# Kernel optimization log

Hardware: AMD Instinct MI355X
Metric: run time of the kernel (lower is better)

The kernel has to match this reference:

```python
import jax, jax.numpy as jnp
import numpy as np

SCORE_THRESHOLD = 0.35
TARGET_CLASS_ID = 0.0
R = 4_194_304  # number of candidate detections (rois)


def setup_inputs() -> dict:
    key = jax.random.key(0)
    k1, k2, k3 = jax.random.split(key, 3)
    class_ids = jax.random.randint(k1, (R,), 0, 4).astype(jnp.float32)
    boxes = jax.random.uniform(k2, (R, 4), dtype=jnp.float32)
    scores = jax.random.uniform(k3, (R,), dtype=jnp.float32)
    detections = jnp.concatenate([class_ids[:, None], boxes, scores[:, None]], axis=1)[None]  # [1, R, 6]
    return {"detections": detections}


def _compact(data, mask):
    # Stable stream compaction with fixed output shape: valid rows moved to the
    # front (original order preserved), invalid tail zero-padded.
    # data: [R, D] float, mask: [R] bool  ->  ([R, D], n_valid)
    order = jnp.argsort(jnp.logical_not(mask), stable=True)  # valid (False-key) first
    sel = jnp.take(data, order, axis=0)
    n = jnp.sum(mask.astype(jnp.int32))
    keep = (jnp.arange(data.shape[0]) < n)[:, None]
    return jnp.where(keep, sel, jnp.zeros((), data.dtype)), n


def reference(detections):
    # detections: [1, R, 6] = [class_id, x1, y1, x2, y2, score]
    d = detections[0]
    class_ids = d[:, 0]
    scores = d[:, 5]
    valid = (class_ids == TARGET_CLASS_ID) & (scores >= SCORE_THRESHOLD)
    valid_full = scores >= SCORE_THRESHOLD

    sel, n = _compact(d, valid)
    # rois: zero class stub + xyxy (score dropped), [1, R, 5]; padded rows are all-zero
    rois = jnp.concatenate([jnp.zeros((d.shape[0], 1), d.dtype), sel[:, 1:5]], axis=1)[None]

    rois_full, n_full = _compact(d, valid_full)
    rois_full = rois_full[None]  # [1, R, 6]

    return rois, rois_full, n, n_full
```

## Files before the change

kernel.cpp:

```cpp
#include <hip/hip_runtime.h>

typedef unsigned int uint32;
typedef unsigned long long uint64;

#define BLOCK 256
#define IPT 16
#define CHUNK (BLOCK * IPT)
#define SCORE_THR 0.35f

__global__ void count_kernel(const float* __restrict__ det,
                             uint32* __restrict__ c0, uint32* __restrict__ c1,
                             int R) {
    int tid = threadIdx.x;
    long long base = (long long)blockIdx.x * CHUNK;
    uint32 cnt0 = 0, cnt1 = 0;
    for (int i = 0; i < IPT; ++i) {
        long long row = base + (long long)i * BLOCK + tid;
        if (row < R) {
            const float* p = det + row * 6;
            float c = p[0];
            float s = p[5];
            bool m1 = (s >= SCORE_THR);
            bool m0 = m1 && (c == 0.0f);
            cnt1 += m1 ? 1u : 0u;
            cnt0 += m0 ? 1u : 0u;
        }
    }
    for (int off = 32; off > 0; off >>= 1) {
        cnt0 += __shfl_down(cnt0, off, 64);
        cnt1 += __shfl_down(cnt1, off, 64);
    }
    __shared__ uint32 r0[BLOCK / 64], r1[BLOCK / 64];
    int wave = tid >> 6, lane = tid & 63;
    if (lane == 0) { r0[wave] = cnt0; r1[wave] = cnt1; }
    __syncthreads();
    if (tid == 0) {
        uint32 t0 = 0, t1 = 0;
        for (int w = 0; w < BLOCK / 64; ++w) { t0 += r0[w]; t1 += r1[w]; }
        c0[blockIdx.x] = t0;
        c1[blockIdx.x] = t1;
    }
}

__global__ void scan_kernel(const uint32* __restrict__ c0, const uint32* __restrict__ c1,
                            uint32* __restrict__ o0, uint32* __restrict__ o1,
                            uint32* __restrict__ totals, float* __restrict__ out_n,
                            int nb) {
    __shared__ uint32 s0[1024], s1[1024];
    int t = threadIdx.x;
    uint32 carry0 = 0, carry1 = 0;
    for (int basei = 0; basei < nb; basei += 1024) {
        int i = basei + t;
        uint32 v0 = (i < nb) ? c0[i] : 0u;
        uint32 v1 = (i < nb) ? c1[i] : 0u;
        s0[t] = v0; s1[t] = v1;
        __syncthreads();
        for (int d = 1; d < 1024; d <<= 1) {
            uint32 a0 = (t >= d) ? s0[t - d] : 0u;
            uint32 a1 = (t >= d) ? s1[t - d] : 0u;
            __syncthreads();
            s0[t] += a0; s1[t] += a1;
            __syncthreads();
        }
        if (i < nb) {
            o0[i] = carry0 + s0[t] - v0;
            o1[i] = carry1 + s1[t] - v1;
        }
        uint32 tot0 = carry0 + s0[1023];
        uint32 tot1 = carry1 + s1[1023];
        __syncthreads();
        carry0 = tot0; carry1 = tot1;
    }
    if (t == 0) {
        totals[0] = carry0;
        totals[1] = carry1;
        out_n[0] = (float)carry0;
        out_n[1] = (float)carry1;
    }
}

__global__ void scatter_kernel(const float* __restrict__ det,
                               float* __restrict__ rois, float* __restrict__ roisf,
                               const uint32* __restrict__ o0, const uint32* __restrict__ o1,
                               int R) {
    __shared__ uint32 wc0[BLOCK / 64], wc1[BLOCK / 64];
    __shared__ uint32 run0, run1;
    int tid = threadIdx.x;
    int wave = tid >> 6, lane = tid & 63;
    if (tid == 0) { run0 = o0[blockIdx.x]; run1 = o1[blockIdx.x]; }
    __syncthreads();
    long long base = (long long)blockIdx.x * CHUNK;
    for (int i = 0; i < IPT; ++i) {
        long long row = base + (long long)i * BLOCK + tid;
        bool m0 = false, m1 = false;
        float d0 = 0, d1 = 0, d2 = 0, d3 = 0, d4 = 0, d5 = 0;
        if (row < R) {
            const float* p = det + row * 6;
            d0 = p[0]; d1 = p[1]; d2 = p[2]; d3 = p[3]; d4 = p[4]; d5 = p[5];
            m1 = (d5 >= SCORE_THR);
            m0 = m1 && (d0 == 0.0f);
        }
        uint64 b0 = __ballot(m0);
        uint64 b1 = __ballot(m1);
        if (lane == 0) { wc0[wave] = (uint32)__popcll(b0); wc1[wave] = (uint32)__popcll(b1); }
        __syncthreads();
        uint32 wp0 = 0, wp1 = 0;
        for (int w = 0; w < wave; ++w) { wp0 += wc0[w]; wp1 += wc1[w]; }
        uint64 lt = (lane == 0) ? 0ull : ((1ull << lane) - 1ull);
        if (m0) {
            uint32 pos = run0 + wp0 + (uint32)__popcll(b0 & lt);
            float* q = rois + (long long)pos * 5;
            q[0] = 0.0f; q[1] = d1; q[2] = d2; q[3] = d3; q[4] = d4;
        }
        if (m1) {
            uint32 pos = run1 + wp1 + (uint32)__popcll(b1 & lt);
            float* q = roisf + (long long)pos * 6;
            q[0] = d0; q[1] = d1; q[2] = d2; q[3] = d3; q[4] = d4; q[5] = d5;
        }
        __syncthreads();
        if (tid == 0) {
            uint32 t0 = 0, t1 = 0;
            for (int w = 0; w < BLOCK / 64; ++w) { t0 += wc0[w]; t1 += wc1[w]; }
            run0 += t0; run1 += t1;
        }
        __syncthreads();
    }
}

__global__ void zero_kernel(float* __restrict__ rois, float* __restrict__ roisf,
                            const uint32* __restrict__ totals, long long R) {
    long long n0 = totals[0], n1 = totals[1];
    long long z0 = R * 5 - n0 * 5;
    long long z1 = R * 6 - n1 * 6;
    long long total = z0 + z1;
    long long idx = (long long)blockIdx.x * blockDim.x + threadIdx.x;
    long long stride = (long long)gridDim.x * blockDim.x;
    float* base0 = rois + n0 * 5;
    float* base1 = roisf + n1 * 6;
    for (long long k = idx; k < total; k += stride) {
        if (k < z0) base0[k] = 0.0f;
        else        base1[k - z0] = 0.0f;
    }
}

extern "C" void kernel_launch(void* const* d_in, const int* in_sizes, int n_in,
                              void* d_out, int out_size, void* d_ws, size_t ws_size,
                              hipStream_t stream) {
    const float* det = (const float*)d_in[0];
    float* out = (float*)d_out;
    int R = in_sizes[0] / 6;
    int NB = (R + CHUNK - 1) / CHUNK;

    uint32* ws = (uint32*)d_ws;
    uint32* c0 = ws;
    uint32* c1 = ws + NB;
    uint32* o0 = ws + 2 * NB;
    uint32* o1 = ws + 3 * NB;
    uint32* totals = ws + 4 * NB;

    float* rois  = out;
    float* roisf = out + (long long)R * 5;
    float* nout  = out + (long long)R * 11;

    count_kernel<<<NB, BLOCK, 0, stream>>>(det, c0, c1, R);
    scan_kernel<<<1, 1024, 0, stream>>>(c0, c1, o0, o1, totals, nout, NB);
    scatter_kernel<<<NB, BLOCK, 0, stream>>>(det, rois, roisf, o0, o1, R);
    zero_kernel<<<2048, BLOCK, 0, stream>>>(rois, roisf, totals, (long long)R);
}
```

Before: 290.9 us.

## Fuse scan, scatter and zero-fill into one kernel with float4 loads

Removes the single-block scan kernel and the separate zero kernel. Each scatter block now sums the per-block counts itself to get its prefix and the totals, then writes compacted rows and zero-fills its share of the padded tail. Both passes load rows as float4 triples covering two rows per thread, and the scatter loop uses double-buffered shared counters so it needs one barrier per iteration instead of three. In exchange, every block redundantly reads all NB counts (1024 blocks) and the zero-fill stride is now tied to the grid size.

```diff
diff --git a/kernel.cpp b/kernel.cpp
--- a/kernel.cpp
+++ b/kernel.cpp
@@ -7,6 +7,21 @@
 #define IPT 16
 #define CHUNK (BLOCK * IPT)
 #define SCORE_THR 0.35f
+
+__device__ inline void block_reduce2(uint32& a, uint32& b) {
+    int tid = threadIdx.x;
+    int wave = tid >> 6, lane = tid & 63;
+    for (int off = 32; off > 0; off >>= 1) {
+        a += __shfl_down(a, off, 64);
+        b += __shfl_down(b, off, 64);
+    }
+    __shared__ uint32 ra[BLOCK / 64], rb[BLOCK / 64];
+    if (lane == 0) { ra[wave] = a; rb[wave] = b; }
+    __syncthreads();
+    uint32 sa = 0, sb = 0;
+    for (int w = 0; w < BLOCK / 64; ++w) { sa += ra[w]; sb += rb[w]; }
+    a = sa; b = sb;
+}
 
 __global__ void count_kernel(const float* __restrict__ det,
                              uint32* __restrict__ c0, uint32* __restrict__ c1,
@@ -14,132 +29,172 @@
     int tid = threadIdx.x;
     long long base = (long long)blockIdx.x * CHUNK;
     uint32 cnt0 = 0, cnt1 = 0;
-    for (int i = 0; i < IPT; ++i) {
-        long long row = base + (long long)i * BLOCK + tid;
-        if (row < R) {
-            const float* p = det + row * 6;
-            float c = p[0];
-            float s = p[5];
-            bool m1 = (s >= SCORE_THR);
-            bool m0 = m1 && (c == 0.0f);
-            cnt1 += m1 ? 1u : 0u;
-            cnt0 += m0 ? 1u : 0u;
-        }
-    }
-    for (int off = 32; off > 0; off >>= 1) {
-        cnt0 += __shfl_down(cnt0, off, 64);
-        cnt1 += __shfl_down(cnt1, off, 64);
-    }
-    __shared__ uint32 r0[BLOCK / 64], r1[BLOCK / 64];
-    int wave = tid >> 6, lane = tid & 63;
-    if (lane == 0) { r0[wave] = cnt0; r1[wave] = cnt1; }
-    __syncthreads();
-    if (tid == 0) {
-        uint32 t0 = 0, t1 = 0;
-        for (int w = 0; w < BLOCK / 64; ++w) { t0 += r0[w]; t1 += r1[w]; }
-        c0[blockIdx.x] = t0;
-        c1[blockIdx.x] = t1;
-    }
-}
-
-__global__ void scan_kernel(const uint32* __restrict__ c0, const uint32* __restrict__ c1,
-                            uint32* __restrict__ o0, uint32* __restrict__ o1,
-                            uint32* __restrict__ totals, float* __restrict__ out_n,
-                            int nb) {
-    __shared__ uint32 s0[1024], s1[1024];
-    int t = threadIdx.x;
-    uint32 carry0 = 0, carry1 = 0;
-    for (int basei = 0; basei < nb; basei += 1024) {
-        int i = basei + t;
-        uint32 v0 = (i < nb) ? c0[i] : 0u;
-        uint32 v1 = (i < nb) ? c1[i] : 0u;
-        s0[t] = v0; s1[t] = v1;
-        __syncthreads();
-        for (int d = 1; d < 1024; d <<= 1) {
-            uint32 a0 = (t >= d) ? s0[t - d] : 0u;
-            uint32 a1 = (t >= d) ? s1[t - d] : 0u;
-            __syncthreads();
-            s0[t] += a0; s1[t] += a1;
-            __syncthreads();
-        }
-        if (i < nb) {
-            o0[i] = carry0 + s0[t] - v0;
-            o1[i] = carry1 + s1[t] - v1;
-        }
-        uint32 tot0 = carry0 + s0[1023];
-        uint32 tot1 = carry1 + s1[1023];
-        __syncthreads();
-        carry0 = tot0; carry1 = tot1;
-    }
-    if (t == 0) {
-        totals[0] = carry0;
-        totals[1] = carry1;
-        out_n[0] = (float)carry0;
-        out_n[1] = (float)carry1;
-    }
-}
-
-__global__ void scatter_kernel(const float* __restrict__ det,
-                               float* __restrict__ rois, float* __restrict__ roisf,
-                               const uint32* __restrict__ o0, const uint32* __restrict__ o1,
-                               int R) {
-    __shared__ uint32 wc0[BLOCK / 64], wc1[BLOCK / 64];
-    __shared__ uint32 run0, run1;
+
+    if (base + CHUNK <= R) {
+        const float4* d4 = (const float4*)det + base * 6 / 4;
+        for (int it = 0; it < IPT / 2; ++it) {
+            const float4* p = d4 + (long long)it * (BLOCK * 3) + 3 * tid;
+            float4 f0 = p[0], f1 = p[1], f2 = p[2];
+            bool mA1 = (f1.y >= SCORE_THR);
+            bool mA0 = mA1 && (f0.x == 0.0f);
+            bool mB1 = (f2.w >= SCORE_THR);
+            bool mB0 = mB1 && (f1.z == 0.0f);
+            cnt1 += (mA1 ? 1u : 0u) + (mB1 ? 1u : 0u);
+            cnt0 += (mA0 ? 1u : 0u) + (mB0 ? 1u : 0u);
+        }
+    } else {
+        for (int i = 0; i < IPT; ++i) {
+            long long row = base + (long long)i * BLOCK + tid;
+            if (row < R) {
+                float c = det[row * 6 + 0];
+                float s = det[row * 6 + 5];
+                bool m1 = (s >= SCORE_THR);
+                bool m0 = m1 && (c == 0.0f);
+                cnt1 += m1 ? 1u : 0u;
+                cnt0 += m0 ? 1u : 0u;
+            }
+        }
+    }
+
+    block_reduce2(cnt0, cnt1);
+    if (tid == 0) { c0[blockIdx.x] = cnt0; c1[blockIdx.x] = cnt1; }
+}
+
+__global__ void scatter_zero_kernel(const float* __restrict__ det,
+                                    float* __restrict__ rois, float* __restrict__ roisf,
+                                    const uint32* __restrict__ c0, const uint32* __restrict__ c1,
+                                    float* __restrict__ out_n,
+                                    int R, int NB) {
     int tid = threadIdx.x;
     int wave = tid >> 6, lane = tid & 63;
-    if (tid == 0) { run0 = o0[blockIdx.x]; run1 = o1[blockIdx.x]; }
+    int bid = blockIdx.x;
+
+    uint32 pre0 = 0, pre1 = 0, tot0 = 0, tot1 = 0;
+    for (int j = tid; j < NB; j += BLOCK) {
+        uint32 a = c0[j], b = c1[j];
+        tot0 += a; tot1 += b;
+        if (j < bid) { pre0 += a; pre1 += b; }
+    }
+    for (int off = 32; off > 0; off >>= 1) {
+        pre0 += __shfl_down(pre0, off, 64);
+        pre1 += __shfl_down(pre1, off, 64);
+        tot0 += __shfl_down(tot0, off, 64);
+        tot1 += __shfl_down(tot1, off, 64);
+    }
+    __shared__ uint32 lp0[4], lp1[4], lt0[4], lt1[4];
+    if (lane == 0) { lp0[wave] = pre0; lp1[wave] = pre1; lt0[wave] = tot0; lt1[wave] = tot1; }
     __syncthreads();
-    long long base = (long long)blockIdx.x * CHUNK;
-    for (int i = 0; i < IPT; ++i) {
-        long long row = base + (long long)i * BLOCK + tid;
-        bool m0 = false, m1 = false;
-        float d0 = 0, d1 = 0, d2 = 0, d3 = 0, d4 = 0, d5 = 0;
-        if (row < R) {
-            const float* p = det + row * 6;
-            d0 = p[0]; d1 = p[1]; d2 = p[2]; d3 = p[3]; d4 = p[4]; d5 = p[5];
-            m1 = (d5 >= SCORE_THR);
-            m0 = m1 && (d0 == 0.0f);
-        }
-        uint64 b0 = __ballot(m0);
-        uint64 b1 = __ballot(m1);
-        if (lane == 0) { wc0[wave] = (uint32)__popcll(b0); wc1[wave] = (uint32)__popcll(b1); }
-        __syncthreads();
-        uint32 wp0 = 0, wp1 = 0;
-        for (int w = 0; w < wave; ++w) { wp0 += wc0[w]; wp1 += wc1[w]; }
-        uint64 lt = (lane == 0) ? 0ull : ((1ull << lane) - 1ull);
-        if (m0) {
-            uint32 pos = run0 + wp0 + (uint32)__popcll(b0 & lt);
-            float* q = rois + (long long)pos * 5;
-            q[0] = 0.0f; q[1] = d1; q[2] = d2; q[3] = d3; q[4] = d4;
-        }
-        if (m1) {
-            uint32 pos = run1 + wp1 + (uint32)__popcll(b1 & lt);
-            float* q = roisf + (long long)pos * 6;
-            q[0] = d0; q[1] = d1; q[2] = d2; q[3] = d3; q[4] = d4; q[5] = d5;
-        }
-        __syncthreads();
-        if (tid == 0) {
-            uint32 t0 = 0, t1 = 0;
-            for (int w = 0; w < BLOCK / 64; ++w) { t0 += wc0[w]; t1 += wc1[w]; }
-            run0 += t0; run1 += t1;
-        }
-        __syncthreads();
-    }
-}
-
-__global__ void zero_kernel(float* __restrict__ rois, float* __restrict__ roisf,
-                            const uint32* __restrict__ totals, long long R) {
-    long long n0 = totals[0], n1 = totals[1];
-    long long z0 = R * 5 - n0 * 5;
-    long long z1 = R * 6 - n1 * 6;
+    pre0 = lp0[0] + lp0[1] + lp0[2] + lp0[3];
+    pre1 = lp1[0] + lp1[1] + lp1[2] + lp1[3];
+    tot0 = lt0[0] + lt0[1] + lt0[2] + lt0[3];
+    tot1 = lt1[0] + lt1[1] + lt1[2] + lt1[3];
+
+    if (bid == 0 && tid == 0) {
+        out_n[0] = (float)tot0;
+        out_n[1] = (float)tot1;
+    }
+
+    __shared__ uint32 wc0[2][4], wc1[2][4];
+    uint32 run0 = pre0, run1 = pre1;
+    long long base = (long long)bid * CHUNK;
+    uint64 ltmask = (1ull << lane) - 1ull;
+
+    if (base + CHUNK <= R) {
+        const float4* d4 = (const float4*)det + base * 6 / 4;
+        for (int it = 0; it < IPT / 2; ++it) {
+            const float4* p = d4 + (long long)it * (BLOCK * 3) + 3 * tid;
+            float4 f0 = p[0], f1 = p[1], f2 = p[2];
+            bool mA1 = (f1.y >= SCORE_THR);
+            bool mA0 = mA1 && (f0.x == 0.0f);
+            bool mB1 = (f2.w >= SCORE_THR);
+            bool mB0 = mB1 && (f1.z == 0.0f);
+
+            uint64 bA0 = __ballot(mA0), bA1 = __ballot(mA1);
+            uint64 bB0 = __ballot(mB0), bB1 = __ballot(mB1);
+
+            int buf = it & 1;
+            if (lane == 0) {
+                wc0[buf][wave] = (uint32)(__popcll(bA0) + __popcll(bB0));
+                wc1[buf][wave] = (uint32)(__popcll(bA1) + __popcll(bB1));
+            }
+            __syncthreads();
+            uint32 wp0 = 0, wp1 = 0, bt0 = 0, bt1 = 0;
+            for (int w = 0; w < 4; ++w) {
+                uint32 a = wc0[buf][w], b = wc1[buf][w];
+                bt0 += a; bt1 += b;
+                if (w < wave) { wp0 += a; wp1 += b; }
+            }
+            uint32 rA0 = run0 + wp0 + (uint32)(__popcll(bA0 & ltmask) + __popcll(bB0 & ltmask));
+            uint32 rB0 = rA0 + (mA0 ? 1u : 0u);
+            uint32 rA1 = run1 + wp1 + (uint32)(__popcll(bA1 & ltmask) + __popcll(bB1 & ltmask));
+            uint32 rB1 = rA1 + (mA1 ? 1u : 0u);
+
+            if (mA0) {
+                float* q = rois + (long long)rA0 * 5;
+                q[0] = 0.0f; q[1] = f0.y; q[2] = f0.z; q[3] = f0.w; q[4] = f1.x;
+            }
+            if (mB0) {
+                float* q = rois + (long long)rB0 * 5;
+                q[0] = 0.0f; q[1] = f1.w; q[2] = f2.x; q[3] = f2.y; q[4] = f2.z;
+            }
+            if (mA1) {
+                float* q = roisf + (long long)rA1 * 6;
+                q[0] = f0.x; q[1] = f0.y; q[2] = f0.z; q[3] = f0.w; q[4] = f1.x; q[5] = f1.y;
+            }
+            if (mB1) {
+                float* q = roisf + (long long)rB1 * 6;
+                q[0] = f1.z; q[1] = f1.w; q[2] = f2.x; q[3] = f2.y; q[4] = f2.z; q[5] = f2.w;
+            }
+            run0 += bt0; run1 += bt1;
+        }
+    } else {
+        for (int i = 0; i < IPT; ++i) {
+            long long row = base + (long long)i * BLOCK + tid;
+            bool m0 = false, m1 = false;
+            float d0 = 0, d1 = 0, d2 = 0, d3 = 0, d4v = 0, d5 = 0;
+            if (row < R) {
+                const float* pp = det + row * 6;
+                d0 = pp[0]; d1 = pp[1]; d2 = pp[2]; d3 = pp[3]; d4v = pp[4]; d5 = pp[5];
+                m1 = (d5 >= SCORE_THR);
+                m0 = m1 && (d0 == 0.0f);
+            }
+            uint64 b0 = __ballot(m0), b1 = __ballot(m1);
+            int buf = i & 1;
+            if (lane == 0) {
+                wc0[buf][wave] = (uint32)__popcll(b0);
+                wc1[buf][wave] = (uint32)__popcll(b1);
+            }
+            __syncthreads();
+            uint32 wp0 = 0, wp1 = 0, bt0 = 0, bt1 = 0;
+            for (int w = 0; w < 4; ++w) {
+                uint32 a = wc0[buf][w], b = wc1[buf][w];
+                bt0 += a; bt1 += b;
+                if (w < wave) { wp0 += a; wp1 += b; }
+            }
+            if (m0) {
+                uint32 pos = run0 + wp0 + (uint32)__popcll(b0 & ltmask);
+                float* q = rois + (long long)pos * 5;
+                q[0] = 0.0f; q[1] = d1; q[2] = d2; q[3] = d3; q[4] = d4v;
+            }
+            if (m1) {
+                uint32 pos = run1 + wp1 + (uint32)__popcll(b1 & ltmask);
+                float* q = roisf + (long long)pos * 6;
+                q[0] = d0; q[1] = d1; q[2] = d2; q[3] = d3; q[4] = d4v; q[5] = d5;
+            }
+            run0 += bt0; run1 += bt1;
+        }
+    }
+
+    long long z0 = (long long)R * 5 - (long long)tot0 * 5;
+    long long z1 = (long long)R * 6 - (long long)tot1 * 6;
     long long total = z0 + z1;
-    long long idx = (long long)blockIdx.x * blockDim.x + threadIdx.x;
-    long long stride = (long long)gridDim.x * blockDim.x;
-    float* base0 = rois + n0 * 5;
-    float* base1 = roisf + n1 * 6;
+    float* zb0 = rois + (long long)tot0 * 5;
+    float* zb1 = roisf + (long long)tot1 * 6;
+    long long idx = (long long)bid * BLOCK + tid;
+    long long stride = (long long)NB * BLOCK;
     for (long long k = idx; k < total; k += stride) {
-        if (k < z0) base0[k] = 0.0f;
-        else        base1[k - z0] = 0.0f;
+        if (k < z0) zb0[k] = 0.0f;
+        else        zb1[k - z0] = 0.0f;
     }
 }
 
@@ -154,16 +209,11 @@
     uint32* ws = (uint32*)d_ws;
     uint32* c0 = ws;
     uint32* c1 = ws + NB;
-    uint32* o0 = ws + 2 * NB;
-    uint32* o1 = ws + 3 * NB;
-    uint32* totals = ws + 4 * NB;
 
     float* rois  = out;
     float* roisf = out + (long long)R * 5;
     float* nout  = out + (long long)R * 11;
 
     count_kernel<<<NB, BLOCK, 0, stream>>>(det, c0, c1, R);
-    scan_kernel<<<1, 1024, 0, stream>>>(c0, c1, o0, o1, totals, nout, NB);
-    scatter_kernel<<<NB, BLOCK, 0, stream>>>(det, rois, roisf, o0, o1, R);
-    zero_kernel<<<2048, BLOCK, 0, stream>>>(rois, roisf, totals, (long long)R);
-}
+    scatter_zero_kernel<<<NB, BLOCK, 0, stream>>>(det, rois, roisf, c0, c1, nout, R, NB);
+}
```

Result: no change. 294.3 us (+1.2%).
